# Optimization experiments

Measured on AMD Instinct MI355X. Metric: run time of the kernel, lower is better.

## Reference

```python
import jax, jax.numpy as jnp
import numpy as np

ALPHA = 0.6
K = 4


def gsdnef_conv(x, edge_index, W, b, alpha, K):
    """SpGSDNEFConv: linear transform then K-step graph-signal-denoising diffusion
    h_{k+1} = (x + alpha * A_hat h_k) / (1 + alpha), A_hat = D^-1/2 (A+I) D^-1/2."""
    n = x.shape[0]
    x = x @ W + b  # [N, C_out]
    loop = jnp.arange(n, dtype=edge_index.dtype)
    src = jnp.concatenate([edge_index[0], loop])
    dst = jnp.concatenate([edge_index[1], loop])
    ones = jnp.ones(src.shape, dtype=x.dtype)
    deg = jax.ops.segment_sum(ones, dst, num_segments=n)
    dinv = jax.lax.rsqrt(jnp.maximum(deg, 1e-12))
    norm = dinv[src] * dinv[dst]  # [E+N]
    inv = 1.0 / (1.0 + alpha)
    h = x
    for _ in range(K):
        agg = jax.ops.segment_sum(h[src] * norm[:, None], dst, num_segments=n)
        h = (x + alpha * agg) * inv
    return h


def setup_inputs() -> dict:
    key = jax.random.key(0)
    ks = jax.random.split(key, 16)
    N, E, C_in, H, C_out = 50000, 800000, 256, 128, 64
    x = jax.random.normal(ks[0], (N, C_in), dtype=jnp.float32)
    edge_index = jax.random.randint(ks[1], (2, E), 0, N, dtype=jnp.int64)

    def lin(k, fan_in, fan_out):
        k1, k2 = jax.random.split(k)
        bound = 1.0 / np.sqrt(fan_in)
        W = jax.random.uniform(k1, (fan_in, fan_out), jnp.float32, -bound, bound)
        b = jax.random.uniform(k2, (fan_out,), jnp.float32, -bound, bound)
        return W, b

    Wc1, bc1 = lin(ks[2], C_in, H)
    Wl1, bl1 = lin(ks[3], C_in, H)
    Wc2, bc2 = lin(ks[4], H, H)
    Wl2, bl2 = lin(ks[5], H, H)
    Wc3, bc3 = lin(ks[6], H, C_out)
    Wl3, bl3 = lin(ks[7], H, C_out)
    return dict(x=x, edge_index=edge_index,
                Wc1=Wc1, bc1=bc1, Wl1=Wl1, bl1=bl1,
                Wc2=Wc2, bc2=bc2, Wl2=Wl2, bl2=bl2,
                Wc3=Wc3, bc3=bc3, Wl3=Wl3, bl3=bl3)


def reference(x, edge_index, Wc1, bc1, Wl1, bl1, Wc2, bc2, Wl2, bl2, Wc3, bc3, Wl3, bl3):
    h = jax.nn.elu(gsdnef_conv(x, edge_index, Wc1, bc1, ALPHA, K) + (x @ Wl1 + bl1))
    h = jax.nn.elu(gsdnef_conv(h, edge_index, Wc2, bc2, ALPHA, K) + (h @ Wl2 + bl2))
    h = gsdnef_conv(h, edge_index, Wc3, bc3, ALPHA, K) + (h @ Wl3 + bl3)
    return h
```

## Files before the change

### kernel.cpp

```cpp
#include <hip/hip_runtime.h>
#include <hip/hip_fp16.h>
#include <math.h>

#define ALPHA_C 0.6f

typedef _Float16 f16;
typedef f16 f16x8 __attribute__((ext_vector_type(8)));
typedef float f32x4 __attribute__((ext_vector_type(4)));

__global__ void detect_idx_kernel(const void* __restrict__ ei, int* __restrict__ flag,
                                  int E, int N) {
    int i = blockIdx.x * blockDim.x + threadIdx.x;
    if (i >= E) return;
    long long v = ((const long long*)ei)[i];
    if (v < 0 || v >= (long long)N) *flag = 1;
}

__global__ void convert_count_kernel(const void* __restrict__ ei, const int* __restrict__ flag,
                                     int* __restrict__ out, int* __restrict__ cnt,
                                     int E, int n2e) {
    int i = blockIdx.x * blockDim.x + threadIdx.x;
    if (i >= n2e) return;
    int v;
    if (*flag == 0)
        v = (int)((const long long*)ei)[i];
    else
        v = ((const int*)ei)[i];
    out[i] = v;
    if (i >= E) atomicAdd(&cnt[v], 1);
}

__global__ void dinv_kernel(const int* __restrict__ cnt, float* __restrict__ dinv, int N) {
    int i = blockIdx.x * blockDim.x + threadIdx.x;
    if (i < N) dinv[i] = rsqrtf((float)cnt[i] + 1.0f);
}

__global__ void block_reduce_kernel(const int* __restrict__ cnt, int* __restrict__ bsum, int n) {
    __shared__ int s[256];
    int tid = threadIdx.x;
    int i = blockIdx.x * 256 + tid;
    int v = (i < n) ? cnt[i] : 0;
    s[tid] = v;
    __syncthreads();
    for (int o = 128; o > 0; o >>= 1) {
        if (tid < o) s[tid] += s[tid + o];
        __syncthreads();
    }
    if (tid == 0) bsum[blockIdx.x] = s[0];
}

__global__ void scan_top_kernel(int* __restrict__ bsum, int nb) {
    __shared__ int s[1024];
    int tid = threadIdx.x;
    int v = (tid < nb) ? bsum[tid] : 0;
    s[tid] = v;
    __syncthreads();
    for (int o = 1; o < 1024; o <<= 1) {
        int t = (tid >= o) ? s[tid - o] : 0;
        __syncthreads();
        s[tid] += t;
        __syncthreads();
    }
    if (tid < nb) bsum[tid] = s[tid] - v;
}

__global__ void scan_fill_kernel(const int* __restrict__ cnt, const int* __restrict__ bsum,
                                 int* __restrict__ row_off, int n) {
    __shared__ int s[256];
    int tid = threadIdx.x;
    int i = blockIdx.x * 256 + tid;
    int v = (i < n) ? cnt[i] : 0;
    s[tid] = v;
    __syncthreads();
    for (int o = 1; o < 256; o <<= 1) {
        int t = (tid >= o) ? s[tid - o] : 0;
        __syncthreads();
        s[tid] += t;
        __syncthreads();
    }
    int base = bsum[blockIdx.x];
    if (i < n) row_off[i] = base + s[tid] - v;
    if (i == n - 1) row_off[n] = base + s[tid];
}

__global__ void fill_kernel(const int* __restrict__ src, const int* __restrict__ dst,
                            const float* __restrict__ dinv, const int* __restrict__ row_off,
                            int* __restrict__ cursor, unsigned int* __restrict__ csre, int E) {
    int e = blockIdx.x * blockDim.x + threadIdx.x;
    if (e >= E) return;
    int d = dst[e], s = src[e];
    int pos = atomicAdd(&cursor[d], 1);
    int idx = row_off[d] + pos;
    float w = dinv[s] * dinv[d];
    csre[idx] = (unsigned int)s |
                ((unsigned int)__half_as_ushort(__float2half(w)) << 16);
}

__global__ void prep_all_w_kernel(
    const float* __restrict__ Wc1, const float* __restrict__ Wl1,
    const float* __restrict__ Wc2, const float* __restrict__ Wl2,
    const float* __restrict__ Wc3, const float* __restrict__ Wl3,
    f16* __restrict__ w1c, f16* __restrict__ w1l,
    f16* __restrict__ w2c, f16* __restrict__ w2l,
    f16* __restrict__ w3c, f16* __restrict__ w3l) {
    int i = blockIdx.x * blockDim.x + threadIdx.x;
    const float* W; f16* O; int K, Nn, base;
    if      (i <  32768) { W = Wc1; O = w1c; K = 256; Nn = 128; base = i; }
    else if (i <  65536) { W = Wl1; O = w1l; K = 256; Nn = 128; base = i - 32768; }
    else if (i <  81920) { W = Wc2; O = w2c; K = 128; Nn = 128; base = i - 65536; }
    else if (i <  98304) { W = Wl2; O = w2l; K = 128; Nn = 128; base = i - 81920; }
    else if (i < 106496) { W = Wc3; O = w3c; K = 128; Nn = 64;  base = i - 98304; }
    else if (i < 114688) { W = Wl3; O = w3l; K = 128; Nn = 64;  base = i - 106496; }
    else return;
    int k = base / Nn, n = base - k * Nn;
    O[(size_t)n * K + k] = (f16)W[base];
}

template <int K, int NH, int AMODE, int SPLIT>
__global__ __launch_bounds__(256) void gemm2_kernel(
    const void* __restrict__ A0v, const void* __restrict__ A1v,
    const f16* __restrict__ WtA, const f16* __restrict__ WtB,
    const float* __restrict__ biasA, const float* __restrict__ biasB,
    f16* __restrict__ CA, f16* __restrict__ CB, int M) {
    constexpr int NT = 2 * NH / 16;
    constexpr int NTS = NT / SPLIT;
    __shared__ f16 Wlds[NTS * 1024];

    int tid = threadIdx.x;
    int wv = tid >> 6, lane = tid & 63;
    int lr = lane & 15, lhi = lane >> 4;
    int m0 = blockIdx.x * 64;
    int tg0 = blockIdx.y * NTS;

    f32x4 acc[NTS];
#pragma unroll
    for (int t = 0; t < NTS; ++t) acc[t] = (f32x4){0.f, 0.f, 0.f, 0.f};

    int arow = m0 + wv * 16 + lr;
    int arow_c = arow < M ? arow : M - 1;
    size_t aoff = (size_t)arow_c * K + lhi * 8;

    for (int k0 = 0; k0 < K; k0 += 64) {
        for (int c = tid; c < NTS * 128; c += 256) {
            int tl = c >> 7;
            int rem = c & 127;
            int ks = rem >> 6, kh = (rem >> 4) & 3, r = rem & 15;
            int tg = tg0 + tl;
            int nloc = (tg < NT / 2) ? tg : tg - NT / 2;
            const f16* srcp = ((tg < NT / 2) ? WtA : WtB)
                              + (size_t)(nloc * 16 + r) * K + k0 + ks * 32 + kh * 8;
            *(f16x8*)&Wlds[(size_t)c * 8] = *(const f16x8*)srcp;
        }
        __syncthreads();

        f16x8 a[2];
#pragma unroll
        for (int ks = 0; ks < 2; ++ks) {
            size_t idx = aoff + k0 + ks * 32;
            if constexpr (AMODE == 0) {
                a[ks] = *(const f16x8*)((const f16*)A0v + idx);
            } else if constexpr (AMODE == 1) {
                const float* xp = (const float*)A0v + idx;
                float4 a0 = *(const float4*)xp;
                float4 a1 = *(const float4*)(xp + 4);
                f16x8 v;
                v[0] = (f16)a0.x; v[1] = (f16)a0.y; v[2] = (f16)a0.z; v[3] = (f16)a0.w;
                v[4] = (f16)a1.x; v[5] = (f16)a1.y; v[6] = (f16)a1.z; v[7] = (f16)a1.w;
                a[ks] = v;
            } else {
                f16x8 u0 = *(const f16x8*)((const f16*)A0v + idx);
                f16x8 u1 = *(const f16x8*)((const f16*)A1v + idx);
                f16x8 v;
#pragma unroll
                for (int j = 0; j < 8; ++j) {
                    float tt = (float)u0[j] + (float)u1[j];
                    v[j] = (f16)(tt > 0.f ? tt : expm1f(tt));
                }
                a[ks] = v;
            }
        }

#pragma unroll
        for (int ks = 0; ks < 2; ++ks) {
#pragma unroll
            for (int t = 0; t < NTS; ++t) {
                f16x8 b = *(const f16x8*)&Wlds[(size_t)(t * 128 + ks * 64 + lane) * 8];
                acc[t] = __builtin_amdgcn_mfma_f32_16x16x32_f16(a[ks], b, acc[t], 0, 0, 0);
            }
        }
        __syncthreads();
    }

    int rbase = m0 + wv * 16 + lhi * 4;
#pragma unroll
    for (int t = 0; t < NTS; ++t) {
        int tg = tg0 + t;
        bool isA = (tg < NT / 2);
        int colg = (isA ? tg : tg - NT / 2) * 16 + lr;
        f16* outp = isA ? CA : CB;
        float bv = (isA ? biasA : biasB)[colg];
#pragma unroll
        for (int r = 0; r < 4; ++r) {
            int row = rbase + r;
            if (row < M) outp[(size_t)row * NH + colg] = (f16)(acc[t][r] + bv);
        }
    }
}

template <int C, bool FINAL>
__global__ __launch_bounds__(256) void diffuse16_kernel(
    const __half* __restrict__ h, const __half* __restrict__ xc,
    const float* __restrict__ dinv, const int* __restrict__ row_off,
    const unsigned int* __restrict__ csre, __half* __restrict__ hout,
    const f16* __restrict__ lin, float* __restrict__ fout, int N) {
    const float inv = 1.0f / (1.0f + ALPHA_C);
    int gid = blockIdx.x * blockDim.x + threadIdx.x;
    int node = gid >> 6;
    if (node >= N) return;
    int lane = threadIdx.x & 63;
    float di = dinv[node];
    float di2 = di * di;
    int e0 = row_off[node], e1 = row_off[node + 1];

    if constexpr (C == 128) {
        int l = lane & 15, grp = lane >> 4;
        float acc[8];
#pragma unroll
        for (int i = 0; i < 8; ++i) acc[i] = 0.f;
        size_t coff = (size_t)l * 8;

        if (grp == 0) {
            float4 rv = *(const float4*)(h + ((size_t)node << 7) + coff);
            const __half2* p = (const __half2*)&rv;
#pragma unroll
            for (int k = 0; k < 4; ++k) {
                float2 f = __half22float2(p[k]);
                acc[2 * k] += di2 * f.x;
                acc[2 * k + 1] += di2 * f.y;
            }
        }
        int e = e0 + grp;
        for (; e + 12 < e1; e += 16) {
            unsigned int ev0 = csre[e], ev1 = csre[e + 4], ev2 = csre[e + 8], ev3 = csre[e + 12];
            float4 r0 = *(const float4*)(h + ((size_t)(ev0 & 0xFFFF) << 7) + coff);
            float4 r1 = *(const float4*)(h + ((size_t)(ev1 & 0xFFFF) << 7) + coff);
            float4 r2 = *(const float4*)(h + ((size_t)(ev2 & 0xFFFF) << 7) + coff);
            float4 r3 = *(const float4*)(h + ((size_t)(ev3 & 0xFFFF) << 7) + coff);
            float w0 = __half2float(__ushort_as_half((unsigned short)(ev0 >> 16)));
            float w1 = __half2float(__ushort_as_half((unsigned short)(ev1 >> 16)));
            float w2 = __half2float(__ushort_as_half((unsigned short)(ev2 >> 16)));
            float w3 = __half2float(__ushort_as_half((unsigned short)(ev3 >> 16)));
            const __half2* p0 = (const __half2*)&r0;
            const __half2* p1 = (const __half2*)&r1;
            const __half2* p2 = (const __half2*)&r2;
            const __half2* p3 = (const __half2*)&r3;
#pragma unroll
            for (int k = 0; k < 4; ++k) {
                float2 f0 = __half22float2(p0[k]);
                float2 f1 = __half22float2(p1[k]);
                float2 f2 = __half22float2(p2[k]);
                float2 f3 = __half22float2(p3[k]);
                acc[2 * k]     += w0 * f0.x + w1 * f1.x + w2 * f2.x + w3 * f3.x;
                acc[2 * k + 1] += w0 * f0.y + w1 * f1.y + w2 * f2.y + w3 * f3.y;
            }
        }
        for (; e < e1; e += 4) {
            unsigned int ev0 = csre[e];
            float4 r0 = *(const float4*)(h + ((size_t)(ev0 & 0xFFFF) << 7) + coff);
            float w0 = __half2float(__ushort_as_half((unsigned short)(ev0 >> 16)));
            const __half2* p0 = (const __half2*)&r0;
#pragma unroll
            for (int k = 0; k < 4; ++k) {
                float2 f0 = __half22float2(p0[k]);
                acc[2 * k]     += w0 * f0.x;
                acc[2 * k + 1] += w0 * f0.y;
            }
        }
#pragma unroll
        for (int i = 0; i < 8; ++i) {
            acc[i] += __shfl_xor(acc[i], 16);
            acc[i] += __shfl_xor(acc[i], 32);
        }
        if (grp == 0) {
            float4 xv = *(const float4*)(xc + ((size_t)node << 7) + coff);
            const __half2* xp = (const __half2*)&xv;
            __half ov[8];
#pragma unroll
            for (int k = 0; k < 4; ++k) {
                float2 xf = __half22float2(xp[k]);
                ov[2 * k]     = __float2half((xf.x + ALPHA_C * acc[2 * k]) * inv);
                ov[2 * k + 1] = __float2half((xf.y + ALPHA_C * acc[2 * k + 1]) * inv);
            }
            *(float4*)(hout + ((size_t)node << 7) + coff) = *(float4*)ov;
        }
    } else {
        int l = lane & 7, grp = lane >> 3;
        float acc[8];
#pragma unroll
        for (int i = 0; i < 8; ++i) acc[i] = 0.f;
        size_t coff = (size_t)l * 8;

        if (grp == 0) {
            float4 rv = *(const float4*)(h + ((size_t)node << 6) + coff);
            const __half2* p = (const __half2*)&rv;
#pragma unroll
            for (int k = 0; k < 4; ++k) {
                float2 f = __half22float2(p[k]);
                acc[2 * k] += di2 * f.x;
                acc[2 * k + 1] += di2 * f.y;
            }
        }
        int e = e0 + grp;
        for (; e + 8 < e1; e += 16) {
            unsigned int ev0 = csre[e], ev1 = csre[e + 8];
            float4 r0 = *(const float4*)(h + ((size_t)(ev0 & 0xFFFF) << 6) + coff);
            float4 r1 = *(const float4*)(h + ((size_t)(ev1 & 0xFFFF) << 6) + coff);
            float w0 = __half2float(__ushort_as_half((unsigned short)(ev0 >> 16)));
            float w1 = __half2float(__ushort_as_half((unsigned short)(ev1 >> 16)));
            const __half2* p0 = (const __half2*)&r0;
            const __half2* p1 = (const __half2*)&r1;
#pragma unroll
            for (int k = 0; k < 4; ++k) {
                float2 f0 = __half22float2(p0[k]);
                float2 f1 = __half22float2(p1[k]);
                acc[2 * k]     += w0 * f0.x + w1 * f1.x;
                acc[2 * k + 1] += w0 * f0.y + w1 * f1.y;
            }
        }
        if (e < e1) {
            unsigned int ev0 = csre[e];
            float4 r0 = *(const float4*)(h + ((size_t)(ev0 & 0xFFFF) << 6) + coff);
            float w0 = __half2float(__ushort_as_half((unsigned short)(ev0 >> 16)));
            const __half2* p0 = (const __half2*)&r0;
#pragma unroll
            for (int k = 0; k < 4; ++k) {
                float2 f0 = __half22float2(p0[k]);
                acc[2 * k]     += w0 * f0.x;
                acc[2 * k + 1] += w0 * f0.y;
            }
        }
#pragma unroll
        for (int i = 0; i < 8; ++i) {
            acc[i] += __shfl_xor(acc[i], 8);
            acc[i] += __shfl_xor(acc[i], 16);
            acc[i] += __shfl_xor(acc[i], 32);
        }
        if (grp == 0) {
            float4 xv = *(const float4*)(xc + ((size_t)node << 6) + coff);
            const __half2* xp = (const __half2*)&xv;
            float r[8];
#pragma unroll
            for (int k = 0; k < 4; ++k) {
                float2 xf = __half22float2(xp[k]);
                r[2 * k]     = (xf.x + ALPHA_C * acc[2 * k]) * inv;
                r[2 * k + 1] = (xf.y + ALPHA_C * acc[2 * k + 1]) * inv;
            }
            if constexpr (FINAL) {
                f16x8 lv = *(const f16x8*)(lin + ((size_t)node << 6) + coff);
                float4 o0, o1;
                o0.x = r[0] + (float)lv[0]; o0.y = r[1] + (float)lv[1];
                o0.z = r[2] + (float)lv[2]; o0.w = r[3] + (float)lv[3];
                o1.x = r[4] + (float)lv[4]; o1.y = r[5] + (float)lv[5];
                o1.z = r[6] + (float)lv[6]; o1.w = r[7] + (float)lv[7];
                float* op = fout + ((size_t)node << 6) + coff;
                *(float4*)op = o0;
                *(float4*)(op + 4) = o1;
            } else {
                __half ov[8];
#pragma unroll
                for (int k = 0; k < 8; ++k) ov[k] = __float2half(r[k]);
                *(float4*)(hout + ((size_t)node << 6) + coff) = *(float4*)ov;
            }
        }
    }
}

extern "C" void kernel_launch(void* const* d_in, const int* in_sizes, int n_in,
                              void* d_out, int out_size, void* d_ws, size_t ws_size,
                              hipStream_t stream) {
    const float* x   = (const float*)d_in[0];
    const void*  ei  = d_in[1];
    const float* Wc1 = (const float*)d_in[2];  const float* bc1 = (const float*)d_in[3];
    const float* Wl1 = (const float*)d_in[4];  const float* bl1 = (const float*)d_in[5];
    const float* Wc2 = (const float*)d_in[6];  const float* bc2 = (const float*)d_in[7];
    const float* Wl2 = (const float*)d_in[8];  const float* bl2 = (const float*)d_in[9];
    const float* Wc3 = (const float*)d_in[10]; const float* bc3 = (const float*)d_in[11];
    const float* Wl3 = (const float*)d_in[12]; const float* bl3 = (const float*)d_in[13];
    float* out = (float*)d_out;

    const int N = in_sizes[0] / 256;
    const int E = in_sizes[1] / 2;

    size_t off = 0;
    auto alloc = [&](size_t bytes) {
        void* p = (char*)d_ws + off;
        off += (bytes + 255) & ~(size_t)255;
        return p;
    };
    f16* B0 = (f16*)alloc((size_t)N * 128 * 2);
    f16* B1 = (f16*)alloc((size_t)N * 128 * 2);
    f16* B2 = (f16*)alloc((size_t)N * 128 * 2);
    f16* B3 = (f16*)alloc((size_t)N * 128 * 2);
    f16* B4 = (f16*)alloc((size_t)N * 128 * 2);
    f16* wt1c = (f16*)alloc((size_t)256 * 128 * 2);
    f16* wt1l = (f16*)alloc((size_t)256 * 128 * 2);
    f16* wt2c = (f16*)alloc((size_t)128 * 128 * 2);
    f16* wt2l = (f16*)alloc((size_t)128 * 128 * 2);
    f16* wt3c = (f16*)alloc((size_t)128 * 64 * 2);
    f16* wt3l = (f16*)alloc((size_t)128 * 64 * 2);
    float* dinv   = (float*)alloc((size_t)N * 4);
    int*   cnt    = (int*)  alloc((size_t)N * 4);
    int*   rowoff = (int*)  alloc((size_t)(N + 1) * 4);
    int*   bsum   = (int*)  alloc(1024 * 4);
    unsigned int* csre = (unsigned int*)alloc((size_t)E * 4);
    int*   idx32  = (int*)  alloc((size_t)2 * E * 4);
    int*   flag   = (int*)  alloc(4);
    int* src32 = idx32;
    int* dst32 = idx32 + E;

    const int TB = 256;
    int ge  = (E + TB - 1) / TB;
    int g2e = (2 * E + TB - 1) / TB;
    int gn  = (N + TB - 1) / TB;
    int nb  = (N + 255) / 256;

    hipMemsetAsync(flag, 0, 4, stream);
    hipMemsetAsync(cnt, 0, (size_t)N * 4, stream);
    detect_idx_kernel<<<ge, TB, 0, stream>>>(ei, flag, E, N);
    convert_count_kernel<<<g2e, TB, 0, stream>>>(ei, flag, idx32, cnt, E, 2 * E);

    dinv_kernel<<<gn, TB, 0, stream>>>(cnt, dinv, N);
    block_reduce_kernel<<<nb, 256, 0, stream>>>(cnt, bsum, N);
    scan_top_kernel<<<1, 1024, 0, stream>>>(bsum, nb);
    scan_fill_kernel<<<nb, 256, 0, stream>>>(cnt, bsum, rowoff, N);
    hipMemsetAsync(cnt, 0, (size_t)N * 4, stream);
    fill_kernel<<<ge, TB, 0, stream>>>(src32, dst32, dinv, rowoff, cnt, csre, E);

    prep_all_w_kernel<<<(114688 + TB - 1) / TB, TB, 0, stream>>>(
        Wc1, Wl1, Wc2, Wl2, Wc3, Wl3, wt1c, wt1l, wt2c, wt2l, wt3c, wt3l);

    dim3 gm((N + 63) / 64, 2);
    int gd = (N * 64 + TB - 1) / TB;

    gemm2_kernel<256, 128, 1, 2><<<gm, TB, 0, stream>>>(x, nullptr, wt1c, wt1l, bc1, bl1, B0, B1, N);
    diffuse16_kernel<128, false><<<gd, TB, 0, stream>>>((__half*)B0, (__half*)B0, dinv, rowoff, csre, (__half*)B2, nullptr, nullptr, N);
    diffuse16_kernel<128, false><<<gd, TB, 0, stream>>>((__half*)B2, (__half*)B0, dinv, rowoff, csre, (__half*)B3, nullptr, nullptr, N);
    diffuse16_kernel<128, false><<<gd, TB, 0, stream>>>((__half*)B3, (__half*)B0, dinv, rowoff, csre, (__half*)B2, nullptr, nullptr, N);
    diffuse16_kernel<128, false><<<gd, TB, 0, stream>>>((__half*)B2, (__half*)B0, dinv, rowoff, csre, (__half*)B3, nullptr, nullptr, N);

    gemm2_kernel<128, 128, 2, 2><<<gm, TB, 0, stream>>>(B3, B1, wt2c, wt2l, bc2, bl2, B0, B4, N);
    diffuse16_kernel<128, false><<<gd, TB, 0, stream>>>((__half*)B0, (__half*)B0, dinv, rowoff, csre, (__half*)B1, nullptr, nullptr, N);
    diffuse16_kernel<128, false><<<gd, TB, 0, stream>>>((__half*)B1, (__half*)B0, dinv, rowoff, csre, (__half*)B2, nullptr, nullptr, N);
    diffuse16_kernel<128, false><<<gd, TB, 0, stream>>>((__half*)B2, (__half*)B0, dinv, rowoff, csre, (__half*)B1, nullptr, nullptr, N);
    diffuse16_kernel<128, false><<<gd, TB, 0, stream>>>((__half*)B1, (__half*)B0, dinv, rowoff, csre, (__half*)B2, nullptr, nullptr, N);

    gemm2_kernel<128, 64, 2, 2><<<gm, TB, 0, stream>>>(B2, B4, wt3c, wt3l, bc3, bl3, B0, B1, N);
    diffuse16_kernel<64, false><<<gd, TB, 0, stream>>>((__half*)B0, (__half*)B0, dinv, rowoff, csre, (__half*)B2, nullptr, nullptr, N);
    diffuse16_kernel<64, false><<<gd, TB, 0, stream>>>((__half*)B2, (__half*)B0, dinv, rowoff, csre, (__half*)B3, nullptr, nullptr, N);
    diffuse16_kernel<64, false><<<gd, TB, 0, stream>>>((__half*)B3, (__half*)B0, dinv, rowoff, csre, (__half*)B2, nullptr, nullptr, N);
    diffuse16_kernel<64, true ><<<gd, TB, 0, stream>>>((__half*)B2, (__half*)B0, dinv, rowoff, csre, nullptr, B1, out, N);
}
```

Baseline: 560.0 us.

## Store features in 32-column blocked layout and map column groups to XCDs

Intermediate feature matrices are now stored column-blocked (groups of 32 channels, each a contiguous N×32 slab). The GEMM reads and writes that layout, and the diffusion kernel processes one 32-channel group per block. Block IDs are mapped so that each XCD works on one column group, which keeps each XCD's gather working set small enough to stay in its local L2. The cost is more passes over the CSR edge list, one per column group, plus strided GEMM stores and a hard-coded assumption of 8 XCDs.

```diff
diff --git a/kernel.cpp b/kernel.cpp
--- a/kernel.cpp
+++ b/kernel.cpp
@@ -138,9 +138,34 @@
 
     int arow = m0 + wv * 16 + lr;
     int arow_c = arow < M ? arow : M - 1;
-    size_t aoff = (size_t)arow_c * K + lhi * 8;
 
     for (int k0 = 0; k0 < K; k0 += 64) {
+        f16x8 a[2];
+#pragma unroll
+        for (int ks = 0; ks < 2; ++ks) {
+            int kk = k0 + ks * 32 + lhi * 8;
+            if constexpr (AMODE == 1) {
+                const float* xp = (const float*)A0v + (size_t)arow_c * K + kk;
+                float4 a0 = *(const float4*)xp;
+                float4 a1 = *(const float4*)(xp + 4);
+                f16x8 v;
+                v[0] = (f16)a0.x; v[1] = (f16)a0.y; v[2] = (f16)a0.z; v[3] = (f16)a0.w;
+                v[4] = (f16)a1.x; v[5] = (f16)a1.y; v[6] = (f16)a1.z; v[7] = (f16)a1.w;
+                a[ks] = v;
+            } else {
+                size_t idx = ((size_t)(kk >> 5) * M + arow_c) * 32 + (kk & 31);
+                f16x8 u0 = *(const f16x8*)((const f16*)A0v + idx);
+                f16x8 u1 = *(const f16x8*)((const f16*)A1v + idx);
+                f16x8 v;
+#pragma unroll
+                for (int j = 0; j < 8; ++j) {
+                    float tt = (float)u0[j] + (float)u1[j];
+                    v[j] = (f16)(tt > 0.f ? tt : expm1f(tt));
+                }
+                a[ks] = v;
+            }
+        }
+
         for (int c = tid; c < NTS * 128; c += 256) {
             int tl = c >> 7;
             int rem = c & 127;
@@ -153,33 +178,6 @@
         }
         __syncthreads();
 
-        f16x8 a[2];
-#pragma unroll
-        for (int ks = 0; ks < 2; ++ks) {
-            size_t idx = aoff + k0 + ks * 32;
-            if constexpr (AMODE == 0) {
-                a[ks] = *(const f16x8*)((const f16*)A0v + idx);
-            } else if constexpr (AMODE == 1) {
-                const float* xp = (const float*)A0v + idx;
-                float4 a0 = *(const float4*)xp;
-                float4 a1 = *(const float4*)(xp + 4);
-                f16x8 v;
-                v[0] = (f16)a0.x; v[1] = (f16)a0.y; v[2] = (f16)a0.z; v[3] = (f16)a0.w;
-                v[4] = (f16)a1.x; v[5] = (f16)a1.y; v[6] = (f16)a1.z; v[7] = (f16)a1.w;
-                a[ks] = v;
-            } else {
-                f16x8 u0 = *(const f16x8*)((const f16*)A0v + idx);
-                f16x8 u1 = *(const f16x8*)((const f16*)A1v + idx);
-                f16x8 v;
-#pragma unroll
-                for (int j = 0; j < 8; ++j) {
-                    float tt = (float)u0[j] + (float)u1[j];
-                    v[j] = (f16)(tt > 0.f ? tt : expm1f(tt));
-                }
-                a[ks] = v;
-            }
-        }
-
 #pragma unroll
         for (int ks = 0; ks < 2; ++ks) {
 #pragma unroll
@@ -199,178 +197,89 @@
         int colg = (isA ? tg : tg - NT / 2) * 16 + lr;
         f16* outp = isA ? CA : CB;
         float bv = (isA ? biasA : biasB)[colg];
+        size_t cbase = ((size_t)(colg >> 5) * M) * 32 + (colg & 31);
 #pragma unroll
         for (int r = 0; r < 4; ++r) {
             int row = rbase + r;
-            if (row < M) outp[(size_t)row * NH + colg] = (f16)(acc[t][r] + bv);
-        }
-    }
-}
-
-template <int C, bool FINAL>
-__global__ __launch_bounds__(256) void diffuse16_kernel(
-    const __half* __restrict__ h, const __half* __restrict__ xc,
+            if (row < M) outp[cbase + (size_t)row * 32] = (f16)(acc[t][r] + bv);
+        }
+    }
+}
+
+template <int NG, bool FINAL>
+__global__ __launch_bounds__(256) void diffuse32_kernel(
+    const f16* __restrict__ h, const f16* __restrict__ xc,
     const float* __restrict__ dinv, const int* __restrict__ row_off,
-    const unsigned int* __restrict__ csre, __half* __restrict__ hout,
+    const unsigned int* __restrict__ csre, f16* __restrict__ hout,
     const f16* __restrict__ lin, float* __restrict__ fout, int N) {
     const float inv = 1.0f / (1.0f + ALPHA_C);
-    int gid = blockIdx.x * blockDim.x + threadIdx.x;
-    int node = gid >> 6;
+    int bid = blockIdx.x;
+    int xcd = bid & 7;
+    int g, idx;
+    if constexpr (NG == 4) { g = xcd >> 1; idx = (bid >> 3) * 2 + (xcd & 1); }
+    else                   { g = xcd >> 2; idx = (bid >> 3) * 4 + (xcd & 3); }
+    int node = idx * 4 + (threadIdx.x >> 6);
     if (node >= N) return;
     int lane = threadIdx.x & 63;
-    float di = dinv[node];
-    float di2 = di * di;
+    int slot = lane >> 2, cl = lane & 3;
+    const f16* hs = h + (size_t)g * N * 32;
+    size_t coff = (size_t)cl * 8;
+    float d = dinv[node];
+    float di2 = d * d;
     int e0 = row_off[node], e1 = row_off[node + 1];
 
-    if constexpr (C == 128) {
-        int l = lane & 15, grp = lane >> 4;
-        float acc[8];
-#pragma unroll
-        for (int i = 0; i < 8; ++i) acc[i] = 0.f;
-        size_t coff = (size_t)l * 8;
-
-        if (grp == 0) {
-            float4 rv = *(const float4*)(h + ((size_t)node << 7) + coff);
-            const __half2* p = (const __half2*)&rv;
-#pragma unroll
-            for (int k = 0; k < 4; ++k) {
-                float2 f = __half22float2(p[k]);
-                acc[2 * k] += di2 * f.x;
-                acc[2 * k + 1] += di2 * f.y;
-            }
-        }
-        int e = e0 + grp;
-        for (; e + 12 < e1; e += 16) {
-            unsigned int ev0 = csre[e], ev1 = csre[e + 4], ev2 = csre[e + 8], ev3 = csre[e + 12];
-            float4 r0 = *(const float4*)(h + ((size_t)(ev0 & 0xFFFF) << 7) + coff);
-            float4 r1 = *(const float4*)(h + ((size_t)(ev1 & 0xFFFF) << 7) + coff);
-            float4 r2 = *(const float4*)(h + ((size_t)(ev2 & 0xFFFF) << 7) + coff);
-            float4 r3 = *(const float4*)(h + ((size_t)(ev3 & 0xFFFF) << 7) + coff);
-            float w0 = __half2float(__ushort_as_half((unsigned short)(ev0 >> 16)));
-            float w1 = __half2float(__ushort_as_half((unsigned short)(ev1 >> 16)));
-            float w2 = __half2float(__ushort_as_half((unsigned short)(ev2 >> 16)));
-            float w3 = __half2float(__ushort_as_half((unsigned short)(ev3 >> 16)));
-            const __half2* p0 = (const __half2*)&r0;
-            const __half2* p1 = (const __half2*)&r1;
-            const __half2* p2 = (const __half2*)&r2;
-            const __half2* p3 = (const __half2*)&r3;
-#pragma unroll
-            for (int k = 0; k < 4; ++k) {
-                float2 f0 = __half22float2(p0[k]);
-                float2 f1 = __half22float2(p1[k]);
-                float2 f2 = __half22float2(p2[k]);
-                float2 f3 = __half22float2(p3[k]);
-                acc[2 * k]     += w0 * f0.x + w1 * f1.x + w2 * f2.x + w3 * f3.x;
-                acc[2 * k + 1] += w0 * f0.y + w1 * f1.y + w2 * f2.y + w3 * f3.y;
-            }
-        }
-        for (; e < e1; e += 4) {
-            unsigned int ev0 = csre[e];
-            float4 r0 = *(const float4*)(h + ((size_t)(ev0 & 0xFFFF) << 7) + coff);
-            float w0 = __half2float(__ushort_as_half((unsigned short)(ev0 >> 16)));
-            const __half2* p0 = (const __half2*)&r0;
-#pragma unroll
-            for (int k = 0; k < 4; ++k) {
-                float2 f0 = __half22float2(p0[k]);
-                acc[2 * k]     += w0 * f0.x;
-                acc[2 * k + 1] += w0 * f0.y;
-            }
-        }
-#pragma unroll
-        for (int i = 0; i < 8; ++i) {
-            acc[i] += __shfl_xor(acc[i], 16);
-            acc[i] += __shfl_xor(acc[i], 32);
-        }
-        if (grp == 0) {
-            float4 xv = *(const float4*)(xc + ((size_t)node << 7) + coff);
-            const __half2* xp = (const __half2*)&xv;
-            __half ov[8];
-#pragma unroll
-            for (int k = 0; k < 4; ++k) {
-                float2 xf = __half22float2(xp[k]);
-                ov[2 * k]     = __float2half((xf.x + ALPHA_C * acc[2 * k]) * inv);
-                ov[2 * k + 1] = __float2half((xf.y + ALPHA_C * acc[2 * k + 1]) * inv);
-            }
-            *(float4*)(hout + ((size_t)node << 7) + coff) = *(float4*)ov;
-        }
-    } else {
-        int l = lane & 7, grp = lane >> 3;
-        float acc[8];
-#pragma unroll
-        for (int i = 0; i < 8; ++i) acc[i] = 0.f;
-        size_t coff = (size_t)l * 8;
-
-        if (grp == 0) {
-            float4 rv = *(const float4*)(h + ((size_t)node << 6) + coff);
-            const __half2* p = (const __half2*)&rv;
-#pragma unroll
-            for (int k = 0; k < 4; ++k) {
-                float2 f = __half22float2(p[k]);
-                acc[2 * k] += di2 * f.x;
-                acc[2 * k + 1] += di2 * f.y;
-            }
-        }
-        int e = e0 + grp;
-        for (; e + 8 < e1; e += 16) {
-            unsigned int ev0 = csre[e], ev1 = csre[e + 8];
-            float4 r0 = *(const float4*)(h + ((size_t)(ev0 & 0xFFFF) << 6) + coff);
-            float4 r1 = *(const float4*)(h + ((size_t)(ev1 & 0xFFFF) << 6) + coff);
-            float w0 = __half2float(__ushort_as_half((unsigned short)(ev0 >> 16)));
-            float w1 = __half2float(__ushort_as_half((unsigned short)(ev1 >> 16)));
-            const __half2* p0 = (const __half2*)&r0;
-            const __half2* p1 = (const __half2*)&r1;
-#pragma unroll
-            for (int k = 0; k < 4; ++k) {
-                float2 f0 = __half22float2(p0[k]);
-                float2 f1 = __half22float2(p1[k]);
-                acc[2 * k]     += w0 * f0.x + w1 * f1.x;
-                acc[2 * k + 1] += w0 * f0.y + w1 * f1.y;
-            }
-        }
-        if (e < e1) {
-            unsigned int ev0 = csre[e];
-            float4 r0 = *(const float4*)(h + ((size_t)(ev0 & 0xFFFF) << 6) + coff);
-            float w0 = __half2float(__ushort_as_half((unsigned short)(ev0 >> 16)));
-            const __half2* p0 = (const __half2*)&r0;
-#pragma unroll
-            for (int k = 0; k < 4; ++k) {
-                float2 f0 = __half22float2(p0[k]);
-                acc[2 * k]     += w0 * f0.x;
-                acc[2 * k + 1] += w0 * f0.y;
-            }
-        }
-#pragma unroll
-        for (int i = 0; i < 8; ++i) {
-            acc[i] += __shfl_xor(acc[i], 8);
-            acc[i] += __shfl_xor(acc[i], 16);
-            acc[i] += __shfl_xor(acc[i], 32);
-        }
-        if (grp == 0) {
-            float4 xv = *(const float4*)(xc + ((size_t)node << 6) + coff);
-            const __half2* xp = (const __half2*)&xv;
-            float r[8];
-#pragma unroll
-            for (int k = 0; k < 4; ++k) {
-                float2 xf = __half22float2(xp[k]);
-                r[2 * k]     = (xf.x + ALPHA_C * acc[2 * k]) * inv;
-                r[2 * k + 1] = (xf.y + ALPHA_C * acc[2 * k + 1]) * inv;
-            }
-            if constexpr (FINAL) {
-                f16x8 lv = *(const f16x8*)(lin + ((size_t)node << 6) + coff);
-                float4 o0, o1;
-                o0.x = r[0] + (float)lv[0]; o0.y = r[1] + (float)lv[1];
-                o0.z = r[2] + (float)lv[2]; o0.w = r[3] + (float)lv[3];
-                o1.x = r[4] + (float)lv[4]; o1.y = r[5] + (float)lv[5];
-                o1.z = r[6] + (float)lv[6]; o1.w = r[7] + (float)lv[7];
-                float* op = fout + ((size_t)node << 6) + coff;
-                *(float4*)op = o0;
-                *(float4*)(op + 4) = o1;
-            } else {
-                __half ov[8];
-#pragma unroll
-                for (int k = 0; k < 8; ++k) ov[k] = __float2half(r[k]);
-                *(float4*)(hout + ((size_t)node << 6) + coff) = *(float4*)ov;
-            }
+    float acc[8];
+#pragma unroll
+    for (int j = 0; j < 8; ++j) acc[j] = 0.f;
+
+    if (slot == 0) {
+        f16x8 sv = *(const f16x8*)(hs + (size_t)node * 32 + coff);
+#pragma unroll
+        for (int j = 0; j < 8; ++j) acc[j] += di2 * (float)sv[j];
+    }
+    int e = e0 + slot;
+    for (; e + 16 < e1; e += 32) {
+        unsigned int ev0 = csre[e], ev1 = csre[e + 16];
+        f16x8 r0 = *(const f16x8*)(hs + (size_t)(ev0 & 0xFFFF) * 32 + coff);
+        f16x8 r1 = *(const f16x8*)(hs + (size_t)(ev1 & 0xFFFF) * 32 + coff);
+        float w0 = __half2float(__ushort_as_half((unsigned short)(ev0 >> 16)));
+        float w1 = __half2float(__ushort_as_half((unsigned short)(ev1 >> 16)));
+#pragma unroll
+        for (int j = 0; j < 8; ++j)
+            acc[j] += w0 * (float)r0[j] + w1 * (float)r1[j];
+    }
+    if (e < e1) {
+        unsigned int ev0 = csre[e];
+        f16x8 r0 = *(const f16x8*)(hs + (size_t)(ev0 & 0xFFFF) * 32 + coff);
+        float w0 = __half2float(__ushort_as_half((unsigned short)(ev0 >> 16)));
+#pragma unroll
+        for (int j = 0; j < 8; ++j) acc[j] += w0 * (float)r0[j];
+    }
+#pragma unroll
+    for (int j = 0; j < 8; ++j) {
+        acc[j] += __shfl_xor(acc[j], 4);
+        acc[j] += __shfl_xor(acc[j], 8);
+        acc[j] += __shfl_xor(acc[j], 16);
+        acc[j] += __shfl_xor(acc[j], 32);
+    }
+    if (slot == 0) {
+        size_t sbase = (size_t)g * N * 32 + (size_t)node * 32 + coff;
+        f16x8 xv = *(const f16x8*)(xc + sbase);
+        if constexpr (FINAL) {
+            f16x8 lv = *(const f16x8*)(lin + sbase);
+            float o[8];
+#pragma unroll
+            for (int j = 0; j < 8; ++j)
+                o[j] = ((float)xv[j] + ALPHA_C * acc[j]) * inv + (float)lv[j];
+            float* op = fout + (size_t)node * 64 + g * 32 + cl * 8;
+            *(float4*)op = *(float4*)&o[0];
+            *(float4*)(op + 4) = *(float4*)&o[4];
+        } else {
+            f16x8 ov;
+#pragma unroll
+            for (int j = 0; j < 8; ++j)
+                ov[j] = (f16)(((float)xv[j] + ALPHA_C * acc[j]) * inv);
+            *(f16x8*)(hout + sbase) = ov;
         }
     }
 }
@@ -440,23 +349,25 @@
         Wc1, Wl1, Wc2, Wl2, Wc3, Wl3, wt1c, wt1l, wt2c, wt2l, wt3c, wt3l);
 
     dim3 gm((N + 63) / 64, 2);
-    int gd = (N * 64 + TB - 1) / TB;
+    int bpg = (N + 3) / 4;
+    int gd4 = ((bpg + 1) / 2) * 8;
+    int gd2 = ((bpg + 3) / 4) * 8;
 
     gemm2_kernel<256, 128, 1, 2><<<gm, TB, 0, stream>>>(x, nullptr, wt1c, wt1l, bc1, bl1, B0, B1, N);
-    diffuse16_kernel<128, false><<<gd, TB, 0, stream>>>((__half*)B0, (__half*)B0, dinv, rowoff, csre, (__half*)B2, nullptr, nullptr, N);
-    diffuse16_kernel<128, false><<<gd, TB, 0, stream>>>((__half*)B2, (__half*)B0, dinv, rowoff, csre, (__half*)B3, nullptr, nullptr, N);
-    diffuse16_kernel<128, false><<<gd, TB, 0, stream>>>((__half*)B3, (__half*)B0, dinv, rowoff, csre, (__half*)B2, nullptr, nullptr, N);
-    diffuse16_kernel<128, false><<<gd, TB, 0, stream>>>((__half*)B2, (__half*)B0, dinv, rowoff, csre, (__half*)B3, nullptr, nullptr, N);
+    diffuse32_kernel<4, false><<<gd4, TB, 0, stream>>>(B0, B0, dinv, rowoff, csre, B2, nullptr, nullptr, N);
+    diffuse32_kernel<4, false><<<gd4, TB, 0, stream>>>(B2, B0, dinv, rowoff, csre, B3, nullptr, nullptr, N);
+    diffuse32_kernel<4, false><<<gd4, TB, 0, stream>>>(B3, B0, dinv, rowoff, csre, B2, nullptr, nullptr, N);
+    diffuse32_kernel<4, false><<<gd4, TB, 0, stream>>>(B2, B0, dinv, rowoff, csre, B3, nullptr, nullptr, N);
 
     gemm2_kernel<128, 128, 2, 2><<<gm, TB, 0, stream>>>(B3, B1, wt2c, wt2l, bc2, bl2, B0, B4, N);
-    diffuse16_kernel<128, false><<<gd, TB, 0, stream>>>((__half*)B0, (__half*)B0, dinv, rowoff, csre, (__half*)B1, nullptr, nullptr, N);
-    diffuse16_kernel<128, false><<<gd, TB, 0, stream>>>((__half*)B1, (__half*)B0, dinv, rowoff, csre, (__half*)B2, nullptr, nullptr, N);
-    diffuse16_kernel<128, false><<<gd, TB, 0, stream>>>((__half*)B2, (__half*)B0, dinv, rowoff, csre, (__half*)B1, nullptr, nullptr, N);
-    diffuse16_kernel<128, false><<<gd, TB, 0, stream>>>((__half*)B1, (__half*)B0, dinv, rowoff, csre, (__half*)B2, nullptr, nullptr, N);
+    diffuse32_kernel<4, false><<<gd4, TB, 0, stream>>>(B0, B0, dinv, rowoff, csre, B1, nullptr, nullptr, N);
+    diffuse32_kernel<4, false><<<gd4, TB, 0, stream>>>(B1, B0, dinv, rowoff, csre, B2, nullptr, nullptr, N);
+    diffuse32_kernel<4, false><<<gd4, TB, 0, stream>>>(B2, B0, dinv, rowoff, csre, B1, nullptr, nullptr, N);
+    diffuse32_kernel<4, false><<<gd4, TB, 0, stream>>>(B1, B0, dinv, rowoff, csre, B2, nullptr, nullptr, N);
 
     gemm2_kernel<128, 64, 2, 2><<<gm, TB, 0, stream>>>(B2, B4, wt3c, wt3l, bc3, bl3, B0, B1, N);
-    diffuse16_kernel<64, false><<<gd, TB, 0, stream>>>((__half*)B0, (__half*)B0, dinv, rowoff, csre, (__half*)B2, nullptr, nullptr, N);
-    diffuse16_kernel<64, false><<<gd, TB, 0, stream>>>((__half*)B2, (__half*)B0, dinv, rowoff, csre, (__half*)B3, nullptr, nullptr, N);
-    diffuse16_kernel<64, false><<<gd, TB, 0, stream>>>((__half*)B3, (__half*)B0, dinv, rowoff, csre, (__half*)B2, nullptr, nullptr, N);
-    diffuse16_kernel<64, true ><<<gd, TB, 0, stream>>>((__half*)B2, (__half*)B0, dinv, rowoff, csre, nullptr, B1, out, N);
-}
+    diffuse32_kernel<2, false><<<gd2, TB, 0, stream>>>(B0, B0, dinv, rowoff, csre, B2, nullptr, nullptr, N);
+    diffuse32_kernel<2, false><<<gd2, TB, 0, stream>>>(B2, B0, dinv, rowoff, csre, B3, nullptr, nullptr, N);
+    diffuse32_kernel<2, false><<<gd2, TB, 0, stream>>>(B3, B0, dinv, rowoff, csre, B2, nullptr, nullptr, N);
+    diffuse32_kernel<2, true ><<<gd2, TB, 0, stream>>>(B2, B0, dinv, rowoff, csre, nullptr, B1, out, N);
+}
```

New measurement: 924.6 us. +65.1%, slower.
